# Kernel optimization log

Measured on AMD Instinct MI355X. Metric: run time of the kernel, lower is better.

Reference implementation:

```python
import jax, jax.numpy as jnp
import numpy as np
import math

D_MODEL = 2048
N_HEADS = 16
D_HEAD = D_MODEL // N_HEADS
MAX_T = 2048
B, T = 2, 2048


def rotate_half(x):
    # interleaved rotate: (x0,x1,x2,x3,...) -> (-x1,x0,-x3,x2,...)
    x1 = x[..., ::2]
    x2 = x[..., 1::2]
    return jnp.stack((-x2, x1), axis=-1).reshape(x.shape)


def setup_inputs() -> dict:
    key = jax.random.key(0)
    k1, k2, k3 = jax.random.split(key, 3)
    x = jax.random.normal(k1, (B, T, D_MODEL), dtype=jnp.float32)
    # torch nn.Linear weights: [out, in]
    s = 1.0 / math.sqrt(D_MODEL)
    Wqkv = jax.random.uniform(k2, (3 * D_MODEL, D_MODEL), dtype=jnp.float32, minval=-s, maxval=s)
    WO = jax.random.uniform(k3, (D_MODEL, D_MODEL), dtype=jnp.float32, minval=-s, maxval=s)
    return {"x": x, "Wqkv": Wqkv, "WO": WO}


def reference(x, Wqkv, WO):
    Bx, Tx, _ = x.shape
    # RoPE tables (buffers)
    pos = jnp.arange(Tx, dtype=jnp.float32)
    freqs = jnp.exp(-math.log(10000.0) * jnp.arange(0, D_HEAD, 2, dtype=jnp.float32) / D_HEAD)
    angles = pos[:, None] * freqs[None, :]               # [T, d_head/2]
    sin = jnp.repeat(jnp.sin(angles), 2, axis=-1)        # [T, d_head]
    cos = jnp.repeat(jnp.cos(angles), 2, axis=-1)
    sin = sin[None, None, :, :]
    cos = cos[None, None, :, :]

    qkv = x @ Wqkv.T                                     # [B, T, 3D]
    q, k, v = jnp.split(qkv, 3, axis=-1)
    def to_heads(t):
        return t.reshape(Bx, Tx, N_HEADS, D_HEAD).transpose(0, 2, 1, 3)  # [B,H,T,d]
    q, k, v = to_heads(q), to_heads(k), to_heads(v)

    q = q * cos + rotate_half(q) * sin
    k = k * cos + rotate_half(k) * sin

    scores = jnp.einsum('bhqd,bhkd->bhqk', q, k) / math.sqrt(D_HEAD)
    mask = jnp.triu(jnp.full((Tx, Tx), -jnp.inf, dtype=scores.dtype), k=1)
    scores = scores + mask
    attn = jax.nn.softmax(scores, axis=-1)
    out = jnp.einsum('bhqk,bhkd->bhqd', attn, v)
    out = out.transpose(0, 2, 1, 3).reshape(Bx, Tx, D_MODEL)
    return out @ WO.T
```

## Files before the change

### kernel.cpp

```cpp
#include <hip/hip_runtime.h>
#include <hip/hip_bf16.h>

typedef unsigned short u16;
typedef __attribute__((ext_vector_type(8))) short bf16x8;
typedef __attribute__((ext_vector_type(4))) float f32x4;

#define B_   2
#define T_   2048
#define DM   2048
#define NH   16
#define DH   128
#define NQKV 6144

__device__ __forceinline__ u16 f2bf(float f) {
  __hip_bfloat16 h = __float2bfloat16(f);
  u16 u; __builtin_memcpy(&u, &h, 2); return u;
}
__device__ __forceinline__ float bf2f(u16 u) {
  __hip_bfloat16 h; __builtin_memcpy(&h, &u, 2); return __bfloat162float(h);
}
__device__ __forceinline__ void gl_lds16(const void* g, void* l) {
  __builtin_amdgcn_global_load_lds(
      (__attribute__((address_space(1))) unsigned int*)g,
      (__attribute__((address_space(3))) unsigned int*)l, 16, 0, 0);
}
__device__ __forceinline__ f32x4 MFMA(bf16x8 a, bf16x8 b, f32x4 c) {
  return __builtin_amdgcn_mfma_f32_16x16x32_bf16(a, b, c, 0, 0, 0);
}

__global__ __launch_bounds__(256) void cast_kernel(const float* __restrict__ in,
                                                   u16* __restrict__ out, int n4) {
  int i = blockIdx.x * 256 + threadIdx.x;
  if (i >= n4) return;
  float4 v = ((const float4*)in)[i];
  ushort4 o;
  o.x = f2bf(v.x); o.y = f2bf(v.y); o.z = f2bf(v.z); o.w = f2bf(v.w);
  ((ushort4*)out)[i] = o;
}

#define G1_M 4096
#define G1_N 6144
#define G1_K 2048

#define MFMA_Q(AQ, M0)                                                        \
  _Pragma("unroll") for (int e_ = 0; e_ < 2; ++e_)                            \
  _Pragma("unroll") for (int n_ = 0; n_ < 4; ++n_)                            \
  _Pragma("unroll") for (int kb_ = 0; kb_ < 2; ++kb_)                         \
    acc[(M0) + e_][n_] = MFMA(AQ[e_][kb_], bfr[n_][kb_], acc[(M0) + e_][n_])

#define BARRIER() asm volatile("s_barrier" ::: "memory")

__global__ __launch_bounds__(512, 2) void gemm1_8ph(const u16* __restrict__ A,
                                                    const u16* __restrict__ Bm,
                                                    u16* __restrict__ C) {
  __shared__ alignas(16) u16 As[2][256 * 64];
  __shared__ alignas(16) u16 Bs[2][256 * 64];
  const int tid = threadIdx.x;
  const int w = tid >> 6, lane = tid & 63;
  const int lrow = lane & 15, quad = lane >> 4;
  const long tileM = (long)blockIdx.y * 256, tileN = (long)blockIdx.x * 256;
  const int wm = (w >> 2) * 128, wn = (w & 3) * 64;

  const int sw8 = w * 8;
  const int srowL = lane >> 3;
  const int schunk = ((lane & 7) ^ srowL) * 8;
  const u16* Ag0 = A + (tileM + sw8 + srowL) * (long)G1_K + schunk;
  const u16* Bg0 = Bm + (tileN + sw8 + srowL) * (long)G1_K + schunk;

  auto stgA = [&](int tt, int h) {
    const int b = tt & 1;
    gl_lds16(Ag0 + (size_t)(h * 128) * G1_K + tt * 64,
             &As[b][(h * 128 + sw8) * 64]);
    gl_lds16(Ag0 + (size_t)(h * 128 + 64) * G1_K + tt * 64,
             &As[b][(h * 128 + 64 + sw8) * 64]);
  };
  auto stgB = [&](int tt, int h) {
    const int b = tt & 1;
    gl_lds16(Bg0 + (size_t)(h * 128) * G1_K + tt * 64,
             &Bs[b][(h * 128 + sw8) * 64]);
    gl_lds16(Bg0 + (size_t)(h * 128 + 64) * G1_K + tt * 64,
             &Bs[b][(h * 128 + 64 + sw8) * 64]);
  };

  const int aBase = (wm + lrow) * 64;
  const int bBase = (wn + lrow) * 64;
  const int slot[2] = { (quad ^ (lrow & 7)) * 8, ((4 + quad) ^ (lrow & 7)) * 8 };

  f32x4 acc[8][4] = {};

  stgA(0, 0); stgA(0, 1); stgB(0, 0); stgB(0, 1);
  stgB(1, 0); stgB(1, 1); stgA(1, 0);
  asm volatile("s_waitcnt vmcnt(6)" ::: "memory");
  BARRIER();

#pragma unroll 1
  for (int t = 0; t < 32; ++t) {
    const u16* AsC = As[t & 1];
    const u16* BsC = Bs[t & 1];
    bf16x8 a01[2][2], a23[2][2], a45[2][2], a67[2][2], bfr[4][2];
#pragma unroll
    for (int e = 0; e < 2; ++e)
#pragma unroll
      for (int kb = 0; kb < 2; ++kb)
        a01[e][kb] = *(const bf16x8*)(AsC + aBase + e * 1024 + slot[kb]);
#pragma unroll
    for (int ni = 0; ni < 4; ++ni)
#pragma unroll
      for (int kb = 0; kb < 2; ++kb)
        bfr[ni][kb] = *(const bf16x8*)(BsC + bBase + ni * 1024 + slot[kb]);
#pragma unroll
    for (int e = 0; e < 2; ++e)
#pragma unroll
      for (int kb = 0; kb < 2; ++kb)
        a23[e][kb] = *(const bf16x8*)(AsC + aBase + (2 + e) * 1024 + slot[kb]);
    if (t + 1 < 32) stgA(t + 1, 1);
    BARRIER();
    __builtin_amdgcn_s_setprio(1);
    MFMA_Q(a01, 0);
    __builtin_amdgcn_s_setprio(0);
    BARRIER();
#pragma unroll
    for (int e = 0; e < 2; ++e)
#pragma unroll
      for (int kb = 0; kb < 2; ++kb) {
        a45[e][kb] = *(const bf16x8*)(AsC + aBase + (4 + e) * 1024 + slot[kb]);
        a67[e][kb] = *(const bf16x8*)(AsC + aBase + (6 + e) * 1024 + slot[kb]);
      }
    if (t + 2 < 32) stgB(t + 2, 0);
    BARRIER();
    __builtin_amdgcn_s_setprio(1);
    MFMA_Q(a23, 2);
    __builtin_amdgcn_s_setprio(0);
    asm volatile("s_waitcnt lgkmcnt(0)" ::: "memory");
    BARRIER();
    if (t + 2 < 32) stgB(t + 2, 1);
    BARRIER();
    __builtin_amdgcn_s_setprio(1);
    MFMA_Q(a45, 4);
    __builtin_amdgcn_s_setprio(0);
    BARRIER();
    if (t + 2 < 32) stgA(t + 2, 0);
    if (t < 30) { asm volatile("s_waitcnt vmcnt(6)" ::: "memory"); }
    else if (t == 30) { asm volatile("s_waitcnt vmcnt(0)" ::: "memory"); }
    BARRIER();
    __builtin_amdgcn_s_setprio(1);
    MFMA_Q(a67, 6);
    __builtin_amdgcn_s_setprio(0);
    BARRIER();
  }

  const long crow = tileM + wm + quad * 4;
  const long ccol = tileN + wn + lrow;
#pragma unroll
  for (int mi = 0; mi < 8; ++mi)
#pragma unroll
    for (int ni = 0; ni < 4; ++ni)
#pragma unroll
      for (int r = 0; r < 4; ++r)
        C[(crow + mi * 16 + r) * (long)G1_N + (ccol + ni * 16)] =
            f2bf(acc[mi][ni][r]);
}

__global__ __launch_bounds__(256) void gemm_bt(const u16* __restrict__ A,
                                               const u16* __restrict__ Bm,
                                               void* __restrict__ Cp,
                                               int M, int N, int K, int out_f32) {
  __shared__ u16 As[128 * 64];
  __shared__ u16 Bs[128 * 64];
  const int tid  = threadIdx.x;
  const int wave = tid >> 6, lane = tid & 63;
  const int lrow = lane & 15, quad = lane >> 4;
  const long tileM = (long)blockIdx.y * 128, tileN = (long)blockIdx.x * 128;
  const int wm = (wave >> 1) * 64, wn = (wave & 1) * 64;
  const int sRowIn = lane >> 3;
  const int sChunk = (lane & 7) ^ sRowIn;
  const int sRow0  = wave * 32 + sRowIn;
  const u16* Ag = A + (tileM + sRow0) * (long)K + sChunk * 8;
  const u16* Bg = Bm + (tileN + sRow0) * (long)K + sChunk * 8;
  u16* AsW = As + wave * 2048;
  u16* BsW = Bs + wave * 2048;
  f32x4 acc[4][4] = {};
  for (int kt = 0; kt < K; kt += 64) {
#pragma unroll
    for (int i = 0; i < 4; ++i)
      gl_lds16(Ag + kt + (size_t)i * 8 * K, AsW + i * 512);
#pragma unroll
    for (int i = 0; i < 4; ++i)
      gl_lds16(Bg + kt + (size_t)i * 8 * K, BsW + i * 512);
    __syncthreads();
#pragma unroll
    for (int kb = 0; kb < 2; ++kb) {
      const int slot8 = (((kb * 4 + quad) ^ (lrow & 7)) * 8);
      bf16x8 af[4], bfr[4];
#pragma unroll
      for (int i = 0; i < 4; ++i)
        af[i]  = *(const bf16x8*)(As + (wm + i * 16 + lrow) * 64 + slot8);
#pragma unroll
      for (int i = 0; i < 4; ++i)
        bfr[i] = *(const bf16x8*)(Bs + (wn + i * 16 + lrow) * 64 + slot8);
#pragma unroll
      for (int mi = 0; mi < 4; ++mi)
#pragma unroll
        for (int ni = 0; ni < 4; ++ni)
          acc[mi][ni] = MFMA(af[mi], bfr[ni], acc[mi][ni]);
    }
    __syncthreads();
  }
  const long crow = tileM + wm + quad * 4;
  const long ccol = tileN + wn + lrow;
  if (out_f32) {
    float* C = (float*)Cp;
#pragma unroll
    for (int mi = 0; mi < 4; ++mi)
#pragma unroll
      for (int ni = 0; ni < 4; ++ni)
#pragma unroll
        for (int r = 0; r < 4; ++r)
          C[(crow + mi * 16 + r) * (long)N + (ccol + ni * 16)] = acc[mi][ni][r];
  } else {
    u16* C = (u16*)Cp;
#pragma unroll
    for (int mi = 0; mi < 4; ++mi)
#pragma unroll
      for (int ni = 0; ni < 4; ++ni)
#pragma unroll
        for (int r = 0; r < 4; ++r)
          C[(crow + mi * 16 + r) * (long)N + (ccol + ni * 16)] = f2bf(acc[mi][ni][r]);
  }
}

__global__ __launch_bounds__(256) void rope_reorder(const u16* __restrict__ qkv,
                                                    u16* __restrict__ Q,
                                                    u16* __restrict__ Kd,
                                                    u16* __restrict__ Vt) {
  const int tt = blockIdx.x;
  const int bh = blockIdx.y;
  const int b = bh >> 4, h = bh & 15;
  const int tid = threadIdx.x;
  __shared__ u16 vlds[64 * 129];
  const float qscale = 0.08838834764831845f;
#pragma unroll
  for (int it = 0; it < 16; ++it) {
    int p  = tid + it * 256;
    int tl = p >> 6;
    int i  = p & 63;
    int t  = tt * 64 + tl;
    float freq  = __expf(-9.210340371976184f * (float)i / 64.0f);
    float angle = (float)t * freq;
    float sn, cs;
    sincosf(angle, &sn, &cs);
    const u16* row = qkv + (size_t)(b * T_ + t) * NQKV;
    size_t qo = ((size_t)bh * T_ + t) * DH + 2 * i;
    float q0 = bf2f(row[h * DH + 2 * i]), q1 = bf2f(row[h * DH + 2 * i + 1]);
    Q[qo]     = f2bf((q0 * cs - q1 * sn) * qscale);
    Q[qo + 1] = f2bf((q1 * cs + q0 * sn) * qscale);
    float k0 = bf2f(row[DM + h * DH + 2 * i]), k1 = bf2f(row[DM + h * DH + 2 * i + 1]);
    Kd[qo]     = f2bf(k0 * cs - k1 * sn);
    Kd[qo + 1] = f2bf(k1 * cs + k0 * sn);
  }
#pragma unroll
  for (int it = 0; it < 32; ++it) {
    int idx = tid + it * 256;
    int tl = idx >> 7, d = idx & 127;
    vlds[tl * 129 + d] =
        qkv[(size_t)(b * T_ + tt * 64 + tl) * NQKV + 2 * DM + h * DH + d];
  }
  __syncthreads();
#pragma unroll
  for (int it = 0; it < 32; ++it) {
    int idx = tid + it * 256;
    int d = idx >> 6, tl = idx & 63;
    Vt[((size_t)bh * DH + d) * T_ + tt * 64 + tl] = vlds[tl * 129 + d];
  }
}

__global__ __launch_bounds__(256) void attn_flash(const u16* __restrict__ Q,
                                                  const u16* __restrict__ K,
                                                  const u16* __restrict__ Vt,
                                                  u16* __restrict__ AO) {
  __shared__ u16 Kl[64 * 128];
  __shared__ u16 Vl[128 * 64];
  __shared__ u16 Pl[4 * 16 * 64];
  const int pairIdx = blockIdx.x;
  const int bh = blockIdx.y;
  const int b = bh >> 4, h = bh & 15;
  const int tid = threadIdx.x;
  const int wave = tid >> 6, lane = tid & 63;
  const int lrow = lane & 15, quad = lane >> 4;
  const u16* Qb = Q + (size_t)bh * T_ * DH;
  const u16* Kb = K + (size_t)bh * T_ * DH;
  const u16* Vb = Vt + (size_t)bh * DH * T_;

  u16* KlW = Kl + wave * 2048;
  u16* VlW = Vl + wave * 2048;
  const int kRowIn = lane >> 4;
  const int vRowIn = lane >> 3;
  const int vChunk = (lane & 7) ^ vRowIn;
  u16* PlW = Pl + wave * 1024;

  for (int pass = 0; pass < 2; ++pass) {
    const int qt = pass == 0 ? (2 * gridDim.x - 1 - pairIdx) : pairIdx;
    const int qbase = qt * 64;

    bf16x8 qf[4];
    {
      const u16* qrow = Qb + (size_t)(qbase + wave * 16 + lrow) * DH + quad * 8;
#pragma unroll
      for (int kc = 0; kc < 4; ++kc) qf[kc] = *(const bf16x8*)(qrow + kc * 32);
    }
    f32x4 o[8] = {};
    float lsum[4] = {0.f, 0.f, 0.f, 0.f};

    for (int j = 0; j <= qt; ++j) {
#pragma unroll
      for (int i = 0; i < 4; ++i) {
        int krow = wave * 16 + i * 4 + kRowIn;
        int kch = (lane & 15) ^ (i * 4 + kRowIn);
        gl_lds16(Kb + (size_t)(j * 64 + krow) * DH + kch * 8, KlW + i * 512);
      }
#pragma unroll
      for (int i = 0; i < 4; ++i) {
        int vd = wave * 32 + i * 8 + vRowIn;
        gl_lds16(Vb + (size_t)vd * T_ + j * 64 + vChunk * 8, VlW + i * 512);
      }
      __syncthreads();

      f32x4 s[4] = {};
#pragma unroll
      for (int kc = 0; kc < 4; ++kc)
#pragma unroll
        for (int ns = 0; ns < 4; ++ns) {
          bf16x8 kf = *(const bf16x8*)(Kl + (ns * 16 + lrow) * 128 +
                                       (((kc * 4 + quad) ^ lrow) * 8));
          s[ns] = MFMA(qf[kc], kf, s[ns]);
        }
      if (j == qt) {
#pragma unroll
        for (int ns = 0; ns < 4; ++ns)
#pragma unroll
          for (int r = 0; r < 4; ++r)
            if (ns * 16 + lrow > wave * 16 + quad * 4 + r) s[ns][r] = -__builtin_inff();
      }
#pragma unroll
      for (int r = 0; r < 4; ++r) {
        const int prow = quad * 4 + r;
#pragma unroll
        for (int ns = 0; ns < 4; ++ns) {
          float p = __expf(s[ns][r]);
          PlW[prow * 64 + (((ns * 2 + (lrow >> 3)) ^ (prow & 7)) * 8) +
              (lrow & 7)] = f2bf(p);
          lsum[r] += p;
        }
      }

#pragma unroll
      for (int kc = 0; kc < 2; ++kc) {
        bf16x8 pf = *(const bf16x8*)(PlW + lrow * 64 +
                                     (((kc * 4 + quad) ^ (lrow & 7)) * 8));
#pragma unroll
        for (int os = 0; os < 8; ++os) {
          bf16x8 vf = *(const bf16x8*)(Vl + (os * 16 + lrow) * 64 +
                                       (((kc * 4 + quad) ^ (lrow & 7)) * 8));
          o[os] = MFMA(pf, vf, o[os]);
        }
      }
      __syncthreads();
    }
#pragma unroll
    for (int r = 0; r < 4; ++r) {
      lsum[r] += __shfl_xor(lsum[r], 1, 16);
      lsum[r] += __shfl_xor(lsum[r], 2, 16);
      lsum[r] += __shfl_xor(lsum[r], 4, 16);
      lsum[r] += __shfl_xor(lsum[r], 8, 16);
    }
#pragma unroll
    for (int r = 0; r < 4; ++r) {
      float inv = 1.0f / lsum[r];
      const size_t row = (size_t)b * T_ + qbase + wave * 16 + quad * 4 + r;
      u16* dst = AO + row * DM + h * DH;
#pragma unroll
      for (int os = 0; os < 8; ++os) dst[os * 16 + lrow] = f2bf(o[os][r] * inv);
    }
  }
}

extern "C" void kernel_launch(void* const* d_in, const int* in_sizes, int n_in,
                              void* d_out, int out_size, void* d_ws, size_t ws_size,
                              hipStream_t stream) {
  const float* x    = (const float*)d_in[0];
  const float* Wqkv = (const float*)d_in[1];
  const float* WO   = (const float*)d_in[2];
  char* ws = (char*)d_ws;
  size_t off = 0;
  u16* xb   = (u16*)(ws + off); off += (size_t)B_ * T_ * DM * 2;
  u16* wqb  = (u16*)(ws + off); off += (size_t)NQKV * DM * 2;
  u16* wob  = (u16*)(ws + off); off += (size_t)DM * DM * 2;
  u16* qkvb = (u16*)(ws + off); off += (size_t)B_ * T_ * NQKV * 2;
  u16* Qb   = (u16*)(ws + off); off += (size_t)B_ * NH * T_ * DH * 2;
  u16* Kb   = (u16*)(ws + off); off += (size_t)B_ * NH * T_ * DH * 2;
  u16* Vtb  = (u16*)(ws + off); off += (size_t)B_ * NH * T_ * DH * 2;
  u16* AO   = xb;

  cast_kernel<<<(B_ * T_ * DM / 4 + 255) / 256, 256, 0, stream>>>(x, xb, B_ * T_ * DM / 4);
  cast_kernel<<<(NQKV * DM / 4 + 255) / 256, 256, 0, stream>>>(Wqkv, wqb, NQKV * DM / 4);
  cast_kernel<<<(DM * DM / 4 + 255) / 256, 256, 0, stream>>>(WO, wob, DM * DM / 4);

  gemm1_8ph<<<dim3(G1_N / 256, G1_M / 256), 512, 0, stream>>>(xb, wqb, qkvb);

  rope_reorder<<<dim3(T_ / 64, B_ * NH), 256, 0, stream>>>(qkvb, Qb, Kb, Vtb);

  attn_flash<<<dim3(T_ / 128, B_ * NH), 256, 0, stream>>>(Qb, Kb, Vtb, AO);

  gemm_bt<<<dim3(DM / 128, B_ * T_ / 128), 256, 0, stream>>>(
      AO, wob, d_out, B_ * T_, DM, DM, 1);
}
```

Measured before the change: 393.9 us.

## Reschedule QKV GEMM phases to reuse one A-fragment register set per phase

Restructures the 8-phase main loop of the QKV projection GEMM. Each phase now loads only its own A fragments into a shared register set, waits on LDS, runs its MFMAs, and then issues the next global-to-LDS stage. Previously A fragments for later phases were prefetched into separate registers. This lowers register pressure, which may help the 2-blocks-per-CU occupancy, but exposes LDS read latency in every phase and adds barriers and lgkmcnt(0) waits.

```diff
diff --git a/kernel.cpp b/kernel.cpp
--- a/kernel.cpp
+++ b/kernel.cpp
@@ -49,6 +49,11 @@
     acc[(M0) + e_][n_] = MFMA(AQ[e_][kb_], bfr[n_][kb_], acc[(M0) + e_][n_])
 
 #define BARRIER() asm volatile("s_barrier" ::: "memory")
+#define LGKM0()                                                               \
+  do {                                                                        \
+    asm volatile("s_waitcnt lgkmcnt(0)" ::: "memory");                        \
+    __builtin_amdgcn_sched_barrier(0);                                        \
+  } while (0)
 
 __global__ __launch_bounds__(512, 2) void gemm1_8ph(const u16* __restrict__ A,
                                                     const u16* __restrict__ Bm,
@@ -97,12 +102,7 @@
   for (int t = 0; t < 32; ++t) {
     const u16* AsC = As[t & 1];
     const u16* BsC = Bs[t & 1];
-    bf16x8 a01[2][2], a23[2][2], a45[2][2], a67[2][2], bfr[4][2];
-#pragma unroll
-    for (int e = 0; e < 2; ++e)
-#pragma unroll
-      for (int kb = 0; kb < 2; ++kb)
-        a01[e][kb] = *(const bf16x8*)(AsC + aBase + e * 1024 + slot[kb]);
+    bf16x8 aF[2][2], bfr[4][2];
 #pragma unroll
     for (int ni = 0; ni < 4; ++ni)
 #pragma unroll
@@ -112,40 +112,51 @@
     for (int e = 0; e < 2; ++e)
 #pragma unroll
       for (int kb = 0; kb < 2; ++kb)
-        a23[e][kb] = *(const bf16x8*)(AsC + aBase + (2 + e) * 1024 + slot[kb]);
+        aF[e][kb] = *(const bf16x8*)(AsC + aBase + e * 1024 + slot[kb]);
+    BARRIER();
+    LGKM0();
+    __builtin_amdgcn_s_setprio(1);
+    MFMA_Q(aF, 0);
+    __builtin_amdgcn_s_setprio(0);
     if (t + 1 < 32) stgA(t + 1, 1);
     BARRIER();
+#pragma unroll
+    for (int e = 0; e < 2; ++e)
+#pragma unroll
+      for (int kb = 0; kb < 2; ++kb)
+        aF[e][kb] = *(const bf16x8*)(AsC + aBase + (2 + e) * 1024 + slot[kb]);
+    BARRIER();
+    LGKM0();
     __builtin_amdgcn_s_setprio(1);
-    MFMA_Q(a01, 0);
+    MFMA_Q(aF, 2);
     __builtin_amdgcn_s_setprio(0);
+    if (t + 2 < 32) stgB(t + 2, 0);
     BARRIER();
 #pragma unroll
     for (int e = 0; e < 2; ++e)
 #pragma unroll
-      for (int kb = 0; kb < 2; ++kb) {
-        a45[e][kb] = *(const bf16x8*)(AsC + aBase + (4 + e) * 1024 + slot[kb]);
-        a67[e][kb] = *(const bf16x8*)(AsC + aBase + (6 + e) * 1024 + slot[kb]);
-      }
-    if (t + 2 < 32) stgB(t + 2, 0);
-    BARRIER();
+      for (int kb = 0; kb < 2; ++kb)
+        aF[e][kb] = *(const bf16x8*)(AsC + aBase + (4 + e) * 1024 + slot[kb]);
+    BARRIER();
+    LGKM0();
     __builtin_amdgcn_s_setprio(1);
-    MFMA_Q(a23, 2);
+    MFMA_Q(aF, 4);
     __builtin_amdgcn_s_setprio(0);
-    asm volatile("s_waitcnt lgkmcnt(0)" ::: "memory");
-    BARRIER();
     if (t + 2 < 32) stgB(t + 2, 1);
     BARRIER();
+#pragma unroll
+    for (int e = 0; e < 2; ++e)
+#pragma unroll
+      for (int kb = 0; kb < 2; ++kb)
+        aF[e][kb] = *(const bf16x8*)(AsC + aBase + (6 + e) * 1024 + slot[kb]);
+    BARRIER();
+    LGKM0();
     __builtin_amdgcn_s_setprio(1);
-    MFMA_Q(a45, 4);
+    MFMA_Q(aF, 6);
     __builtin_amdgcn_s_setprio(0);
-    BARRIER();
     if (t + 2 < 32) stgA(t + 2, 0);
     if (t < 30) { asm volatile("s_waitcnt vmcnt(6)" ::: "memory"); }
     else if (t == 30) { asm volatile("s_waitcnt vmcnt(0)" ::: "memory"); }
-    BARRIER();
-    __builtin_amdgcn_s_setprio(1);
-    MFMA_Q(a67, 6);
-    __builtin_amdgcn_s_setprio(0);
     BARRIER();
   }
 
```

New measurement: 414.6 us. 5.2% more time.
